# Kernel tuning notes

Hardware: AMD Instinct MI355X
Metric: run time of the kernel (lower is better)

## Reference

```python
import jax, jax.numpy as jnp
import numpy as np
import math

B, S, D, H, L, DF = 16, 512, 512, 8, 6, 2048
DK = D // H
EPS = 1e-6


def _xavier(key, shape):
    # xavier_uniform over the last two dims (matches nn.init.xavier_uniform_)
    fan_in, fan_out = shape[-2], shape[-1]
    lim = math.sqrt(6.0 / (fan_in + fan_out))
    return jax.random.uniform(key, shape, jnp.float32, -lim, lim)


def setup_inputs() -> dict:
    key = jax.random.key(0)
    ks = jax.random.split(key, 12)
    return {
        "x": jax.random.normal(ks[0], (B, S, D), jnp.float32),
        "pe_table": jax.random.normal(ks[1], (S, D), jnp.float32),  # _4by8_pe weight
        "pe_q_w": _xavier(ks[2], (D, D)), "pe_q_b": jnp.zeros((D,), jnp.float32),
        "pe_k_w": _xavier(ks[3], (D, D)), "pe_k_b": jnp.zeros((D,), jnp.float32),
        "Wq": _xavier(ks[4], (L, D, D)), "bq": jnp.zeros((L, D), jnp.float32),
        "Wk": _xavier(ks[5], (L, D, D)), "bk": jnp.zeros((L, D), jnp.float32),
        "Wv": _xavier(ks[6], (L, D, D)), "bv": jnp.zeros((L, D), jnp.float32),
        "Wo": _xavier(ks[7], (L, D, D)), "bo": jnp.zeros((L, D), jnp.float32),
        "ln1_g": jnp.ones((L, D), jnp.float32), "ln1_b": jnp.zeros((L, D), jnp.float32),
        "W1": _xavier(ks[8], (L, D, DF)), "b1": jnp.zeros((L, DF), jnp.float32),
        "W2": _xavier(ks[9], (L, DF, D)), "b2": jnp.zeros((L, D), jnp.float32),
        "ln2_g": jnp.ones((L, D), jnp.float32), "ln2_b": jnp.zeros((L, D), jnp.float32),
    }


def _layernorm(y, g, b):
    m = jnp.mean(y, axis=-1, keepdims=True)
    v = jnp.var(y, axis=-1, keepdims=True)  # biased, as torch LayerNorm
    return (y - m) * jax.lax.rsqrt(v + EPS) * g + b


def reference(x, pe_table, pe_q_w, pe_q_b, pe_k_w, pe_k_b,
              Wq, bq, Wk, bk, Wv, bv, Wo, bo,
              ln1_g, ln1_b, W1, b1, W2, b2, ln2_g, ln2_b):
    scale = math.sqrt(2 * DK)
    h = x * math.sqrt(D)

    # scores_pe is identical for every batch element (pe_onehot = arange repeated)
    pq = (pe_table @ pe_q_w + pe_q_b).reshape(S, H, DK).transpose(1, 0, 2)  # [H,S,dk]
    pk = (pe_table @ pe_k_w + pe_k_b).reshape(S, H, DK).transpose(1, 0, 2)  # [H,S,dk]
    scores_pe = jnp.einsum('hqd,hkd->hqk', pq, pk) / scale  # [H,S,S]

    def step(h, p):
        wq, bq_, wk, bk_, wv, bv_, wo, bo_, g1, gb1, w1, fb1, w2, fb2, g2, gb2 = p
        q = (h @ wq + bq_).reshape(B, S, H, DK).transpose(0, 2, 1, 3)  # [B,H,S,dk]
        k = (h @ wk + bk_).reshape(B, S, H, DK).transpose(0, 2, 1, 3)
        v = (h @ wv + bv_).reshape(B, S, H, DK).transpose(0, 2, 1, 3)
        scores = jnp.einsum('bhqd,bhkd->bhqk', q, k) / scale + scores_pe  # [B,H,S,S]
        attn = jax.nn.softmax(scores, axis=-1)
        o = jnp.einsum('bhqk,bhkd->bhqd', attn, v).transpose(0, 2, 1, 3).reshape(B, S, D)
        o = o @ wo + bo_
        h1 = _layernorm(o + h, g1, gb1)
        f = jax.nn.gelu(h1 @ w1 + fb1, approximate=False) @ w2 + fb2
        h2 = _layernorm(f + h1, g2, gb2)
        return h2, None

    params = (Wq, bq, Wk, bk, Wv, bv, Wo, bo, ln1_g, ln1_b, W1, b1, W2, b2, ln2_g, ln2_b)
    h, _ = jax.lax.scan(step, h, params)
    pe_out = jnp.broadcast_to(pe_table, (B, S, D))
    return h, pe_out
```

## Files before the change

kernel.cpp:

```cpp
#include <hip/hip_runtime.h>
#include <hip/hip_bf16.h>

typedef __hip_bfloat16 bf16;
typedef short bf16x8 __attribute__((ext_vector_type(8)));
typedef float f32x4 __attribute__((ext_vector_type(4)));

#define DEV static __device__ __forceinline__

DEV f32x4 fzero4(){ f32x4 z; z[0]=0.f; z[1]=0.f; z[2]=0.f; z[3]=0.f; return z; }

DEV float bf2f(bf16 v){
  unsigned int u = ((unsigned int)*(unsigned short*)&v) << 16;
  return *(float*)&u;
}
DEV float bf2s(short s){
  unsigned int u = ((unsigned int)(unsigned short)s) << 16;
  return *(float*)&u;
}

DEV void gl2lds16(const bf16* g, bf16* l){
  __builtin_amdgcn_global_load_lds(
    (const __attribute__((address_space(1))) void*)g,
    (__attribute__((address_space(3))) void*)l, 16, 0, 0);
}

enum { EP_F32=0, EP_BF16=1, EP_GELU=2, EP_HILO=3, EP_QKV=4 };

template<int EPI, int NMT>
__global__ __launch_bounds__(256) void gemm_bt(
    const bf16* A0, const bf16* A1, const bf16* A2,
    const bf16* B0, const bf16* B1, const bf16* B2,
    int npass, int lda, int ldb, int M, int N, int K,
    const float* __restrict__ bs0, const float* __restrict__ bs1, const float* __restrict__ bs2,
    float alpha, void* o0, void* o1, void* o2,
    int nn, int mchunk, int azs, int bzs, int ozs)
{
  constexpr int BM = NMT*32;
  __shared__ __align__(16) bf16 As[2][BM*32];
  __shared__ __align__(16) bf16 Bs[2][128*32];
  const int t = threadIdx.x;
  const int lane = t & 63;
  const int w = t >> 6;
  const int wr = w >> 1, wc = w & 1;
  const int bid = blockIdx.x;
  const int xcd = bid & 7;
  const int idx = bid >> 3;
  const int qm = idx / nn;
  const int mb = xcd*mchunk + qm;
  const int nb = idx - qm*nn;
  const int m0 = mb*BM, n0 = nb*128;
  const int l15 = lane & 15, l4 = lane >> 4;
  const int grow = (lane >> 2);
  const int gcol = (lane & 3) * 8;
  const int z = blockIdx.z;
  if (azs){ A0 += (size_t)z*azs; if(A1) A1 += (size_t)z*azs; if(A2) A2 += (size_t)z*azs; }
  if (bzs){ B0 += (size_t)z*bzs; if(B1) B1 += (size_t)z*bzs; if(B2) B2 += (size_t)z*bzs; }

  auto Aof = [&](int p){ return (p==0)?A0:((p==1)?A1:A2); };
  auto Bof = [&](int p){ return (p==0)?B0:((p==1)?B1:B2); };

  auto stageAB = [&](int cb, const bf16* Ag, const bf16* Bg, int k0){
    if constexpr (NMT==4){
      #pragma unroll
      for (int q=0;q<2;q++){
        int row = w*32 + q*16 + grow;
        gl2lds16(Ag + (size_t)(m0+row)*lda + k0 + gcol, As[cb] + (w*32+q*16)*32);
        gl2lds16(Bg + (size_t)(n0+row)*ldb + k0 + gcol, Bs[cb] + (w*32+q*16)*32);
      }
    } else {
      int rA = w*16 + grow;
      gl2lds16(Ag + (size_t)(m0+rA)*lda + k0 + gcol, As[cb] + w*16*32);
      #pragma unroll
      for (int sb=0;sb<2;sb++){
        int rB = (2*w+sb)*16 + grow;
        gl2lds16(Bg + (size_t)(n0+rB)*ldb + k0 + gcol, Bs[cb] + (2*w+sb)*16*32);
      }
    }
  };

  f32x4 acc[NMT][4];
  #pragma unroll
  for (int i=0;i<NMT;i++)
    #pragma unroll
    for (int j=0;j<4;j++) acc[i][j] = fzero4();

  int cur = 0;
  stageAB(0, A0, B0, 0);
  for (int p=0;p<npass;p++){
    for (int k0=0;k0<K;k0+=32){
      __syncthreads();
      int kn = k0 + 32;
      if (kn < K)            stageAB(cur^1, Aof(p), Bof(p), kn);
      else if (p+1 < npass)  stageAB(cur^1, Aof(p+1), Bof(p+1), 0);
      bf16x8 af[NMT], bfv[4];
      #pragma unroll
      for (int mt=0;mt<NMT;mt++) af[mt] = *(const bf16x8*)(As[cur] + (wr*(NMT*16)+mt*16+l15)*32 + 8*l4);
      #pragma unroll
      for (int nt=0;nt<4;nt++) bfv[nt] = *(const bf16x8*)(Bs[cur] + (wc*64+nt*16+l15)*32 + 8*l4);
      #pragma unroll
      for (int mt=0;mt<NMT;mt++)
        #pragma unroll
        for (int nt=0;nt<4;nt++)
          acc[mt][nt] = __builtin_amdgcn_mfma_f32_16x16x32_bf16(af[mt], bfv[nt], acc[mt][nt], 0, 0, 0);
      cur ^= 1;
    }
  }

  #pragma unroll
  for (int mt=0;mt<NMT;mt++){
    #pragma unroll
    for (int nt=0;nt<4;nt++){
      const int crow = m0 + wr*(NMT*16) + mt*16 + l4*4;
      const int ccol = n0 + wc*64 + nt*16 + l15;
      #pragma unroll
      for (int j=0;j<4;j++){
        float v = acc[mt][nt][j];
        int r = crow + j;
        if (EPI==EP_F32){
          float b = bs0 ? bs0[ccol] : 0.f;
          ((float*)o0)[(size_t)r*N + ccol] = alpha*v + b;
        } else if (EPI==EP_BF16){
          float b = bs0 ? bs0[ccol] : 0.f;
          ((bf16*)o0 + (size_t)z*ozs)[(size_t)r*N + ccol] = __float2bfloat16(alpha*v + b);
        } else if (EPI==EP_GELU){
          float xx = v + bs0[ccol];
          float g = 0.5f*xx*(1.f + erff(xx*0.70710678118654752f));
          ((bf16*)o0)[(size_t)r*N + ccol] = __float2bfloat16(g);
        } else if (EPI==EP_HILO){
          float xx = (v + bs0[ccol]) * alpha;
          bf16 hi = __float2bfloat16(xx);
          ((bf16*)o0)[(size_t)r*N + ccol] = hi;
          ((bf16*)o1)[(size_t)r*N + ccol] = __float2bfloat16(xx - bf2f(hi));
        } else {
          int n = ccol;
          if (n < 512){
            ((bf16*)o0)[(size_t)r*512 + n] = __float2bfloat16((v + bs0[n]) * alpha);
          } else if (n < 1024){
            ((bf16*)o1)[(size_t)r*512 + (n-512)] = __float2bfloat16(v + bs1[n-512]);
          } else {
            int d = n - 1024;
            int bb = r >> 9, s = r & 511;
            int hh = d >> 6, dd = d & 63;
            ((bf16*)o2)[(size_t)(((bb*8)+hh)*64 + dd)*512 + s] = __float2bfloat16(v + bs2[d]);
          }
        }
      }
    }
  }
}

template<int SPLIT>
__global__ __launch_bounds__(256) void attn_mfma(
  const bf16* __restrict__ Q, const bf16* __restrict__ Qlo,
  const bf16* __restrict__ Kh, const bf16* __restrict__ Klo,
  const bf16* __restrict__ VT, const bf16* __restrict__ SPE,
  bf16* __restrict__ O)
{
  __shared__ __align__(16) bf16 K_lds[64*64];
  __shared__ __align__(16) bf16 V_lds[64*64];
  __shared__ __align__(16) bf16 Klo_lds[SPLIT ? 64*64 : 8];
  __shared__ __align__(16) bf16 P_lds[4][16*64];
  const int t = threadIdx.x;
  const int lane = t & 63, w = t >> 6;
  const int l15 = lane & 15, l4 = lane >> 4;
  const int bid = blockIdx.x;
  const int h = bid & 7;
  const int s2 = bid >> 3;
  const int b = s2 >> 3, qblk = s2 & 7;
  const int q0 = qblk*64 + w*16;
  const float inv_scale = 0.08838834764831845f;
  const int xorv = (l15 & 7) << 3;

  bf16x8 qf[2], qflo[2];
  #pragma unroll
  for (int kst=0;kst<2;kst++){
    qf[kst] = *(const bf16x8*)(Q + (size_t)(b*512 + q0 + l15)*512 + h*64 + kst*32 + 8*l4);
    if (SPLIT) qflo[kst] = *(const bf16x8*)(Qlo + (size_t)(b*512 + q0 + l15)*512 + h*64 + kst*32 + 8*l4);
  }
  f32x4 accO[4];
  #pragma unroll
  for (int dt=0;dt<4;dt++) accO[dt] = fzero4();
  float mrow[4], lrow[4];
  #pragma unroll
  for (int j=0;j<4;j++){ mrow[j] = -1e30f; lrow[j] = 0.f; }

  const bf16* spe_h = SPE + (size_t)h*262144;
  const bf16* vbase = VT + (size_t)((b*8)+h)*32768;

  for (int n0=0;n0<512;n0+=64){
    #pragma unroll
    for (int st=0;st<2;st++){
      int rl = w*16 + st*8 + (lane>>3);
      int jj = (lane&7) ^ (rl&7);
      gl2lds16(Kh + (size_t)(b*512 + n0 + rl)*512 + h*64 + jj*8, K_lds + (w*16+st*8)*64);
      if (SPLIT)
        gl2lds16(Klo + (size_t)(b*512 + n0 + rl)*512 + h*64 + jj*8, Klo_lds + (w*16+st*8)*64);
      gl2lds16(vbase + (size_t)rl*512 + n0 + jj*8, V_lds + (w*16+st*8)*64);
    }
    __syncthreads();

    f32x4 sc[4];
    #pragma unroll
    for (int c=0;c<4;c++) sc[c] = fzero4();
    #pragma unroll
    for (int c=0;c<4;c++){
      const int rr = c*16 + l15;
      #pragma unroll
      for (int kst=0;kst<2;kst++){
        bf16x8 kf = *(const bf16x8*)(K_lds + rr*64 + ((kst*32 + 8*l4) ^ xorv));
        sc[c] = __builtin_amdgcn_mfma_f32_16x16x32_bf16(qf[kst], kf, sc[c], 0,0,0);
        if (SPLIT){
          sc[c] = __builtin_amdgcn_mfma_f32_16x16x32_bf16(qflo[kst], kf, sc[c], 0,0,0);
          bf16x8 kfl = *(const bf16x8*)(Klo_lds + rr*64 + ((kst*32 + 8*l4) ^ xorv));
          sc[c] = __builtin_amdgcn_mfma_f32_16x16x32_bf16(qf[kst], kfl, sc[c], 0,0,0);
        }
      }
    }
    float sv[4][4];
    #pragma unroll
    for (int c=0;c<4;c++)
      #pragma unroll
      for (int j=0;j<4;j++){
        int qr = q0 + l4*4 + j;
        sv[c][j] = sc[c][j]*inv_scale + bf2f(spe_h[(size_t)qr*512 + n0 + c*16 + l15]);
      }
    float fac[4];
    #pragma unroll
    for (int j=0;j<4;j++){
      float m2 = fmaxf(fmaxf(sv[0][j],sv[1][j]), fmaxf(sv[2][j],sv[3][j]));
      m2 = fmaxf(m2, __shfl_xor(m2,1));
      m2 = fmaxf(m2, __shfl_xor(m2,2));
      m2 = fmaxf(m2, __shfl_xor(m2,4));
      m2 = fmaxf(m2, __shfl_xor(m2,8));
      float mn = fmaxf(mrow[j], m2);
      fac[j] = __expf(mrow[j] - mn);
      mrow[j] = mn;
    }
    #pragma unroll
    for (int j=0;j<4;j++){
      int row = l4*4 + j;
      float ts = 0.f;
      #pragma unroll
      for (int c=0;c<4;c++){
        float pv = __expf(sv[c][j] - mrow[j]);
        ts += pv;
        P_lds[w][row*64 + ((c*16 + l15) ^ ((row&7)<<3))] = __float2bfloat16(pv);
      }
      ts += __shfl_xor(ts,1); ts += __shfl_xor(ts,2);
      ts += __shfl_xor(ts,4); ts += __shfl_xor(ts,8);
      lrow[j] = lrow[j]*fac[j] + ts;
      #pragma unroll
      for (int dt=0;dt<4;dt++) accO[dt][j] *= fac[j];
    }
    #pragma unroll
    for (int kv=0;kv<2;kv++){
      bf16x8 pf = *(const bf16x8*)(P_lds[w] + l15*64 + ((kv*32 + 8*l4) ^ xorv));
      #pragma unroll
      for (int dt=0;dt<4;dt++){
        const int d = dt*16 + l15;
        bf16x8 vf = *(const bf16x8*)(V_lds + d*64 + ((kv*32 + 8*l4) ^ xorv));
        accO[dt] = __builtin_amdgcn_mfma_f32_16x16x32_bf16(pf, vf, accO[dt], 0,0,0);
      }
    }
    __syncthreads();
  }
  #pragma unroll
  for (int dt=0;dt<4;dt++)
    #pragma unroll
    for (int j=0;j<4;j++){
      float v = accO[dt][j] / lrow[j];
      int r = q0 + l4*4 + j;
      O[(size_t)(b*512+r)*512 + h*64 + dt*16 + l15] = __float2bfloat16(v);
    }
}

__global__ __launch_bounds__(256) void ln_kernel(
  const bf16* __restrict__ tmp, const float* __restrict__ resid,
  const float* __restrict__ g, const float* __restrict__ bta,
  float* __restrict__ outf, bf16* __restrict__ outb)
{
  const int row = blockIdx.x*4 + (threadIdx.x>>6);
  const int lane = threadIdx.x & 63;
  const size_t base = (size_t)row*512 + lane*8;
  bf16x8 a = *(const bf16x8*)(tmp+base);
  float4 r0 = *(const float4*)(resid+base), r1 = *(const float4*)(resid+base+4);
  float x[8];
  x[0]=bf2s(a[0])+r0.x; x[1]=bf2s(a[1])+r0.y;
  x[2]=bf2s(a[2])+r0.z; x[3]=bf2s(a[3])+r0.w;
  x[4]=bf2s(a[4])+r1.x; x[5]=bf2s(a[5])+r1.y;
  x[6]=bf2s(a[6])+r1.z; x[7]=bf2s(a[7])+r1.w;
  float s=0.f, sq=0.f;
  #pragma unroll
  for (int i=0;i<8;i++){ s += x[i]; sq += x[i]*x[i]; }
  #pragma unroll
  for (int d=1; d<64; d<<=1){ s += __shfl_xor(s,d); sq += __shfl_xor(sq,d); }
  float mean = s*(1.f/512.f);
  float var = sq*(1.f/512.f) - mean*mean;
  float rr = rsqrtf(var + 1e-6f);
  #pragma unroll
  for (int i=0;i<8;i++){
    int d = lane*8 + i;
    float y = (x[i]-mean)*rr*g[d] + bta[d];
    outf[base+i] = y;
    outb[base+i] = __float2bfloat16(y);
  }
}

template<bool LO>
__global__ __launch_bounds__(256) void tcast(
  const float* __restrict__ src, int srcStride,
  bf16* __restrict__ dst, int dstStride, bf16* __restrict__ dlo,
  int R, int C)
{
  __shared__ float tile[32][33];
  const int z = blockIdx.z;
  src += (size_t)z*srcStride;
  dst += (size_t)z*dstStride;
  const int tx = threadIdx.x & 31, ty = threadIdx.x >> 5;
  const int r0 = blockIdx.y*32, c0 = blockIdx.x*32;
  #pragma unroll
  for (int p=0;p<4;p++)
    tile[ty+8*p][tx] = src[(size_t)(r0+ty+8*p)*C + c0+tx];
  __syncthreads();
  #pragma unroll
  for (int p=0;p<4;p++){
    float v = tile[tx][ty+8*p];
    bf16 hi = __float2bfloat16(v);
    dst[(size_t)(c0+ty+8*p)*R + r0+tx] = hi;
    if (LO) dlo[(size_t)(c0+ty+8*p)*R + r0+tx] = __float2bfloat16(v - bf2f(hi));
  }
}

__global__ void castbf(const float* __restrict__ in, bf16* __restrict__ out, int n){
  int i = blockIdx.x*blockDim.x + threadIdx.x;
  if (i < n) out[i] = __float2bfloat16(in[i]);
}

__global__ void init_h(const float* __restrict__ x, float* __restrict__ hf,
                       bf16* __restrict__ hb, bf16* __restrict__ hlo, int n){
  int i = blockIdx.x*blockDim.x + threadIdx.x;
  if (i < n){
    float v = x[i]*22.627416997969522f;
    hf[i] = v;
    bf16 hi = __float2bfloat16(v);
    hb[i] = hi;
    hlo[i] = __float2bfloat16(v - bf2f(hi));
  }
}

__global__ void pe_out(const float* __restrict__ pe, float* __restrict__ out, int n1){
  int i = blockIdx.x*blockDim.x + threadIdx.x;
  if (i < n1) out[n1 + i] = pe[i & 262143];
}

extern "C" void kernel_launch(void* const* d_in, const int* in_sizes, int n_in,
                              void* d_out, int out_size, void* d_ws, size_t ws_size,
                              hipStream_t stream)
{
  const float* x    = (const float*)d_in[0];
  const float* pe   = (const float*)d_in[1];
  const float* peqw = (const float*)d_in[2];
  const float* peqb = (const float*)d_in[3];
  const float* pekw = (const float*)d_in[4];
  const float* pekb = (const float*)d_in[5];
  const float* Wq   = (const float*)d_in[6];
  const float* bq   = (const float*)d_in[7];
  const float* Wk   = (const float*)d_in[8];
  const float* bk   = (const float*)d_in[9];
  const float* Wv   = (const float*)d_in[10];
  const float* bv   = (const float*)d_in[11];
  const float* Wo   = (const float*)d_in[12];
  const float* bo   = (const float*)d_in[13];
  const float* g1   = (const float*)d_in[14];
  const float* bb1  = (const float*)d_in[15];
  const float* W1   = (const float*)d_in[16];
  const float* fb1  = (const float*)d_in[17];
  const float* W2   = (const float*)d_in[18];
  const float* fb2  = (const float*)d_in[19];
  const float* g2   = (const float*)d_in[20];
  const float* bb2  = (const float*)d_in[21];

  char* wp = (char*)d_ws;
  auto carve = [&](size_t bytes)->void*{ void* r = (void*)wp; wp += (bytes + 255) & ~(size_t)255; return r; };
  float* hf   = (float*)carve(16777216);
  float* h1f  = (float*)carve(16777216);
  char*  regB = (char*)carve(16777216);
  bf16*  tmpb = (bf16*)regB;
  bf16*  qlo  = (bf16*)regB;
  bf16*  klo  = (bf16*)(regB + 8388608);
  bf16* hb    = (bf16*)carve(8388608);
  bf16* hlo   = (bf16*)carve(8388608);
  bf16* h1b   = (bf16*)carve(8388608);
  char* regA  = (char*)carve(33554432);
  bf16* gbuf  = (bf16*)regA;
  bf16* qb    = (bf16*)regA;
  bf16* kbuf  = (bf16*)(regA + 8388608);
  bf16* vT    = (bf16*)(regA + 16777216);
  bf16* obuf  = (bf16*)(regA + 25165824);
  bf16* WqkvT = (bf16*)carve(9437184);
  bf16* WoT   = (bf16*)carve(3145728);
  bf16* W1T   = (bf16*)carve(12582912);
  bf16* W2T   = (bf16*)carve(12582912);
  bf16* Wq0h  = (bf16*)carve(524288);
  bf16* Wq0l  = (bf16*)carve(524288);
  bf16* Wk0h  = (bf16*)carve(524288);
  bf16* Wk0l  = (bf16*)carve(524288);
  bf16* peb   = (bf16*)carve(524288);
  bf16* pqwT  = (bf16*)carve(524288);
  bf16* pkwT  = (bf16*)carve(524288);
  bf16* pqb   = (bf16*)carve(524288);
  bf16* pkb   = (bf16*)carve(524288);
  bf16* spe   = (bf16*)carve(4194304);

  dim3 B256(256);
  const float INV_SCALE = 0.08838834764831845f;

  tcast<false><<<dim3(16,16,6),B256,0,stream>>>(Wq, 262144, WqkvT,          786432, nullptr, 512, 512);
  tcast<false><<<dim3(16,16,6),B256,0,stream>>>(Wk, 262144, WqkvT + 262144, 786432, nullptr, 512, 512);
  tcast<false><<<dim3(16,16,6),B256,0,stream>>>(Wv, 262144, WqkvT + 524288, 786432, nullptr, 512, 512);
  tcast<false><<<dim3(16,16,6),B256,0,stream>>>(Wo, 262144, WoT, 262144, nullptr, 512, 512);
  tcast<false><<<dim3(64,16,6),B256,0,stream>>>(W1, 1048576, W1T, 1048576, nullptr, 512, 2048);
  tcast<false><<<dim3(16,64,6),B256,0,stream>>>(W2, 1048576, W2T, 1048576, nullptr, 2048, 512);
  tcast<false><<<dim3(16,16,1),B256,0,stream>>>(peqw, 262144, pqwT, 262144, nullptr, 512, 512);
  tcast<false><<<dim3(16,16,1),B256,0,stream>>>(pekw, 262144, pkwT, 262144, nullptr, 512, 512);
  tcast<true ><<<dim3(16,16,1),B256,0,stream>>>(Wq, 262144, Wq0h, 262144, Wq0l, 512, 512);
  tcast<true ><<<dim3(16,16,1),B256,0,stream>>>(Wk, 262144, Wk0h, 262144, Wk0l, 512, 512);
  castbf<<<1024,B256,0,stream>>>(pe, peb, 262144);
  init_h<<<16384,B256,0,stream>>>(x, hf, hb, hlo, 4194304);

  gemm_bt<EP_BF16,2><<<dim3(32),B256,0,stream>>>(peb,nullptr,nullptr, pqwT,nullptr,nullptr, 1, 512,512, 512,512,512, peqb,nullptr,nullptr, 1.f, pqb,nullptr,nullptr, 4,1, 0,0,0);
  gemm_bt<EP_BF16,2><<<dim3(32),B256,0,stream>>>(peb,nullptr,nullptr, pkwT,nullptr,nullptr, 1, 512,512, 512,512,512, pekb,nullptr,nullptr, 1.f, pkb,nullptr,nullptr, 4,1, 0,0,0);
  gemm_bt<EP_BF16,2><<<dim3(32,1,8),B256,0,stream>>>(pqb,nullptr,nullptr, pkb,nullptr,nullptr, 1, 512,512, 512,512,64, nullptr,nullptr,nullptr, INV_SCALE, spe,nullptr,nullptr, 4,1, 64,64,262144);

  for (int l=0;l<6;l++){
    const bf16* WQKV = WqkvT + l*786432;
    const float* bql = bq + l*512;
    const float* bkl = bk + l*512;
    const float* bvl = bv + l*512;
    gemm_bt<EP_QKV,4><<<dim3(768),B256,0,stream>>>(hb,nullptr,nullptr, WQKV,nullptr,nullptr, 1, 512,512, 8192,1536,512, bql,bkl,bvl, 1.f, qb, kbuf, vT, 12,8, 0,0,0);
    if (l==0){
      gemm_bt<EP_HILO,2><<<dim3(512),B256,0,stream>>>(hb,hb,hlo, Wq0h,Wq0l,Wq0h, 3, 512,512, 8192,512,512, bql,nullptr,nullptr, 1.f, qb, qlo, nullptr, 4,16, 0,0,0);
      gemm_bt<EP_HILO,2><<<dim3(512),B256,0,stream>>>(hb,hb,hlo, Wk0h,Wk0l,Wk0h, 3, 512,512, 8192,512,512, bkl,nullptr,nullptr, 1.f, kbuf, klo, nullptr, 4,16, 0,0,0);
      attn_mfma<1><<<dim3(1024),B256,0,stream>>>(qb,qlo,kbuf,klo,vT,spe,obuf);
    } else {
      attn_mfma<0><<<dim3(1024),B256,0,stream>>>(qb,qb,kbuf,kbuf,vT,spe,obuf);
    }
    gemm_bt<EP_BF16,2><<<dim3(512),B256,0,stream>>>(obuf,nullptr,nullptr, WoT+l*262144,nullptr,nullptr, 1, 512,512, 8192,512,512, bo+l*512,nullptr,nullptr, 1.f, tmpb,nullptr,nullptr, 4,16, 0,0,0);
    ln_kernel<<<2048,B256,0,stream>>>(tmpb, hf, g1+l*512, bb1+l*512, h1f, h1b);
    gemm_bt<EP_GELU,4><<<dim3(1024),B256,0,stream>>>(h1b,nullptr,nullptr, W1T+l*1048576,nullptr,nullptr, 1, 512,512, 8192,2048,512, fb1+l*2048,nullptr,nullptr, 1.f, gbuf,nullptr,nullptr, 16,8, 0,0,0);
    gemm_bt<EP_BF16,2><<<dim3(512),B256,0,stream>>>(gbuf,nullptr,nullptr, W2T+l*1048576,nullptr,nullptr, 1, 2048,2048, 8192,512,2048, fb2+l*512,nullptr,nullptr, 1.f, tmpb,nullptr,nullptr, 4,16, 0,0,0);
    ln_kernel<<<2048,B256,0,stream>>>(tmpb, h1f, g2+l*512, bb2+l*512,
                                      (l==5) ? (float*)d_out : hf, hb);
  }
  pe_out<<<16384,B256,0,stream>>>(pe, (float*)d_out, 4194304);
}
```

Baseline: 1.284 ms.

## Triple-buffer GEMM LDS staging with explicit vmcnt waits and single barrier

The GEMM main loop moves from double to triple LDS buffering and flattens the pass and K loops into one stage loop. Each step now issues the load for stage s+2 and waits with a partial s_waitcnt vmcnt, so one stage's global-to-LDS loads stay in flight across the barrier. Before, __syncthreads effectively drained all outstanding loads every iteration. The cost is 50% more shared memory per block, which may lower occupancy, and the hand-coded vmcnt counts must match the number of loads issued per stage.

```diff
diff --git a/kernel.cpp b/kernel.cpp
--- a/kernel.cpp
+++ b/kernel.cpp
@@ -36,8 +36,8 @@
     int nn, int mchunk, int azs, int bzs, int ozs)
 {
   constexpr int BM = NMT*32;
-  __shared__ __align__(16) bf16 As[2][BM*32];
-  __shared__ __align__(16) bf16 Bs[2][128*32];
+  __shared__ __align__(16) bf16 As[3][BM*32];
+  __shared__ __align__(16) bf16 Bs[3][128*32];
   const int t = threadIdx.x;
   const int lane = t & 63;
   const int w = t >> 6;
@@ -59,7 +59,14 @@
   auto Aof = [&](int p){ return (p==0)?A0:((p==1)?A1:A2); };
   auto Bof = [&](int p){ return (p==0)?B0:((p==1)?B1:B2); };
 
-  auto stageAB = [&](int cb, const bf16* Ag, const bf16* Bg, int k0){
+  const int kpp = K >> 5;
+  const int nst = npass * kpp;
+
+  auto stageS = [&](int cb, int s){
+    int p = s / kpp;
+    int k0 = (s - p*kpp) << 5;
+    const bf16* Ag = Aof(p);
+    const bf16* Bg = Bof(p);
     if constexpr (NMT==4){
       #pragma unroll
       for (int q=0;q<2;q++){
@@ -84,26 +91,31 @@
     #pragma unroll
     for (int j=0;j<4;j++) acc[i][j] = fzero4();
 
-  int cur = 0;
-  stageAB(0, A0, B0, 0);
-  for (int p=0;p<npass;p++){
-    for (int k0=0;k0<K;k0+=32){
-      __syncthreads();
-      int kn = k0 + 32;
-      if (kn < K)            stageAB(cur^1, Aof(p), Bof(p), kn);
-      else if (p+1 < npass)  stageAB(cur^1, Aof(p+1), Bof(p+1), 0);
-      bf16x8 af[NMT], bfv[4];
-      #pragma unroll
-      for (int mt=0;mt<NMT;mt++) af[mt] = *(const bf16x8*)(As[cur] + (wr*(NMT*16)+mt*16+l15)*32 + 8*l4);
-      #pragma unroll
-      for (int nt=0;nt<4;nt++) bfv[nt] = *(const bf16x8*)(Bs[cur] + (wc*64+nt*16+l15)*32 + 8*l4);
-      #pragma unroll
-      for (int mt=0;mt<NMT;mt++)
-        #pragma unroll
-        for (int nt=0;nt<4;nt++)
-          acc[mt][nt] = __builtin_amdgcn_mfma_f32_16x16x32_bf16(af[mt], bfv[nt], acc[mt][nt], 0, 0, 0);
-      cur ^= 1;
-    }
+  stageS(0, 0);
+  if (nst > 1) stageS(1, 1);
+  for (int s=0; s<nst; ++s){
+    if (s == nst-1){
+      asm volatile("s_waitcnt vmcnt(0)" ::: "memory");
+    } else if constexpr (NMT==4){
+      asm volatile("s_waitcnt vmcnt(4)" ::: "memory");
+    } else {
+      asm volatile("s_waitcnt vmcnt(3)" ::: "memory");
+    }
+    __builtin_amdgcn_s_barrier();
+    asm volatile("" ::: "memory");
+    if (s+2 < nst) stageS((s+2)%3, s+2);
+    const int cb = s % 3;
+    bf16x8 af[NMT], bfv[4];
+    #pragma unroll
+    for (int mt=0;mt<NMT;mt++) af[mt] = *(const bf16x8*)(As[cb] + (wr*(NMT*16)+mt*16+l15)*32 + 8*l4);
+    #pragma unroll
+    for (int nt=0;nt<4;nt++) bfv[nt] = *(const bf16x8*)(Bs[cb] + (wc*64+nt*16+l15)*32 + 8*l4);
+    #pragma unroll
+    for (int mt=0;mt<NMT;mt++)
+      #pragma unroll
+      for (int nt=0;nt<4;nt++)
+        acc[mt][nt] = __builtin_amdgcn_mfma_f32_16x16x32_bf16(af[mt], bfv[nt], acc[mt][nt], 0, 0, 0);
+    asm volatile("" ::: "memory");
   }
 
   #pragma unroll
@@ -139,9 +151,9 @@
             ((bf16*)o1)[(size_t)r*512 + (n-512)] = __float2bfloat16(v + bs1[n-512]);
           } else {
             int d = n - 1024;
-            int bb = r >> 9, s = r & 511;
+            int bb = r >> 9, s2 = r & 511;
             int hh = d >> 6, dd = d & 63;
-            ((bf16*)o2)[(size_t)(((bb*8)+hh)*64 + dd)*512 + s] = __float2bfloat16(v + bs2[d]);
+            ((bf16*)o2)[(size_t)(((bb*8)+hh)*64 + dd)*512 + s2] = __float2bfloat16(v + bs2[d]);
           }
         }
       }
```

After: 1.316 ms. 2.5% more time.
